# Performance work log

Measured on AMD Instinct MI355X. Metric: run time of the kernel, lower is better.

## Reference

```python
import jax, jax.numpy as jnp
import numpy as np

BETA = 0.2
ALPHA_NEG = 0.8
ALPHA_POS = 0.2
EPS = 1e-8  # torch cosine_similarity eps

B, D, P = 8192, 256, 4096


def setup_inputs() -> dict:
    key = jax.random.key(0)
    k1, k2 = jax.random.split(key)
    embeddings = jax.random.normal(k1, (B, D), dtype=jnp.float32)
    positive_pairs = jax.random.randint(k2, (P, 2), 0, B, dtype=jnp.int32)
    return {"embeddings": embeddings, "positive_pairs": positive_pairs}


def reference(embeddings, positive_pairs):
    b = embeddings.shape[0]
    p = positive_pairs.shape[0]
    # cosine similarity matrix (normalize once, single GEMM)
    nrm = jnp.maximum(jnp.linalg.norm(embeddings, axis=1, keepdims=True), EPS)
    e = embeddings / nrm
    cos = e @ e.T                              # [B, B]
    exp_cos = jnp.exp(cos / BETA)
    ii = positive_pairs[:, 0]
    jj = positive_pairs[:, 1]
    # mask = eye + positive pairs (both directions)
    mask = jnp.eye(b, dtype=bool)
    mask = mask.at[ii, jj].set(True).at[jj, ii].set(True)
    exp_masked = jnp.where(mask, 0.0, exp_cos)  # masked_fill(mask, 0)
    pos_ij = exp_cos[ii, jj]                   # [P]
    pos_ji = exp_cos[jj, ii]                   # [P]
    exp_i = exp_masked[ii]                     # [P, B]
    exp_j = exp_masked[jj]                     # [P, B]
    # hard-negative mining via alpha_neg quantile per row
    thr_i = jnp.quantile(exp_i, ALPHA_NEG, axis=1, keepdims=True)
    thr_j = jnp.quantile(exp_j, ALPHA_NEG, axis=1, keepdims=True)
    S_i = jnp.sum(jnp.where(exp_i >= thr_i, exp_i, 0.0), axis=1)  # [P]
    S_j = jnp.sum(jnp.where(exp_j >= thr_j, exp_j, 0.0), axis=1)  # [P]
    # hard-positive mining via alpha_pos quantile
    thr_pij = jnp.quantile(pos_ij, ALPHA_POS)
    thr_pji = jnp.quantile(pos_ji, ALPHA_POS)
    sel_ij = pos_ij <= thr_pij
    sel_ji = pos_ji <= thr_pji
    # torch loop zips the two (order-preserving) boolean-selected lists ->
    # truncates to min count; values are never cross-coupled, only the count.
    kmin = jnp.minimum(sel_ij.sum(), sel_ji.sum())
    act_ij = sel_ij & ((jnp.cumsum(sel_ij.astype(jnp.int32)) - 1) < kmin)
    act_ji = sel_ji & ((jnp.cumsum(sel_ji.astype(jnp.int32)) - 1) < kmin)
    # -log(pk / (pk + S[m])) = log1p(S[m] / pk), summed over all m per pk
    term_ij = jnp.log1p(S_i[None, :] / pos_ij[:, None])  # [P, P]
    term_ji = jnp.log1p(S_j[None, :] / pos_ji[:, None])  # [P, P]
    loss = (jnp.sum(term_ij * act_ij[:, None].astype(term_ij.dtype))
            + jnp.sum(term_ji * act_ji[:, None].astype(term_ji.dtype)))
    return loss / (2.0 * p)
```

## Files before the change

kernel.cpp:

```cpp
#include <hip/hip_runtime.h>
#include <stdint.h>

#define BN    8192
#define DK    256
#define PN    4096
#define MAXP  16
#define RANK_ASC 6553
#define QSTEP 0.02f

typedef float f32x4  __attribute__((ext_vector_type(4)));
typedef int   i32x4  __attribute__((ext_vector_type(4)));

__device__ __forceinline__ void gload_lds16(const void* g, void* l) {
  __builtin_amdgcn_global_load_lds(
      (const __attribute__((address_space(1))) unsigned int*)g,
      (__attribute__((address_space(3))) unsigned int*)l, 16, 0, 0);
}

__device__ __forceinline__ void find_bin_256(const unsigned* hist, int rank,
                                             int* sh, unsigned* wtot) {
  const int tid = threadIdx.x, lane = tid & 63, w = tid >> 6;
  unsigned x = hist[tid];
  unsigned pref = x;
  #pragma unroll
  for (int o = 1; o < 64; o <<= 1) {
    unsigned y = __shfl_up(pref, o);
    if (lane >= o) pref += y;
  }
  if (lane == 63) wtot[w] = pref;
  __syncthreads();
  unsigned woff = 0;
  for (int i = 0; i < w; ++i) woff += wtot[i];
  unsigned incl = pref + woff, excl = incl - x;
  if ((unsigned)rank >= excl && (unsigned)rank < incl) { sh[0] = tid; sh[1] = rank - (int)excl; }
  __syncthreads();
}

__device__ __forceinline__ float block_sum4(float x, float* red4) {
  const int lane = threadIdx.x & 63, w = threadIdx.x >> 6;
  #pragma unroll
  for (int o = 32; o; o >>= 1) x += __shfl_xor(x, o);
  __syncthreads();
  if (lane == 0) red4[w] = x;
  __syncthreads();
  return red4[0] + red4[1] + red4[2] + red4[3];
}

__global__ void __launch_bounds__(256) norm_pairs_kernel(
    const float* __restrict__ X, signed char* __restrict__ Ei8,
    const int2* __restrict__ pairs, int* pcount, int* partners,
    int* rowlist, int* cnt) {
  const int tid  = threadIdx.x;
  const int lane = tid & 63;
  const int wib  = tid >> 6;
  const int row  = blockIdx.x * 4 + wib;

  float4 x = ((const float4*)(X + (size_t)row * DK))[lane];
  float ss = x.x * x.x + x.y * x.y + x.z * x.z + x.w * x.w;
  #pragma unroll
  for (int o = 32; o; o >>= 1) ss += __shfl_xor(ss, o);
  float inv = 127.0f / fmaxf(sqrtf(ss), 1e-8f);
  int c0 = (int)rintf(inv * x.x);
  int c1 = (int)rintf(inv * x.y);
  int c2 = (int)rintf(inv * x.z);
  int c3 = (int)rintf(inv * x.w);
  unsigned u = (unsigned)(c0 & 255) | ((unsigned)(c1 & 255) << 8)
             | ((unsigned)(c2 & 255) << 16) | ((unsigned)(c3 & 255) << 24);
  ((unsigned*)(Ei8 + (size_t)row * DK))[lane] = u;

  const int p = blockIdx.x * 256 + tid;
  if (p < PN) {
    int2 pr = pairs[p];
    int ix = atomicAdd(&pcount[pr.x], 1);
    if (ix == 0) { int q = atomicAdd(cnt, 1); rowlist[q] = pr.x; }
    if (ix < MAXP) partners[pr.x * MAXP + ix] = pr.y;
    int iy = atomicAdd(&pcount[pr.y], 1);
    if (iy == 0) { int q = atomicAdd(cnt, 1); rowlist[q] = pr.y; }
    if (iy < MAXP) partners[pr.y * MAXP + iy] = pr.x;
  }
}

__global__ void __launch_bounds__(256) pos_kernel(
    const signed char* __restrict__ Ei8, const int2* __restrict__ pairs,
    float* __restrict__ pos) {
  const int tid  = threadIdx.x;
  const int lane = tid & 63;
  const int wib  = tid >> 6;
  const int p    = blockIdx.x * 4 + wib;
  int2 pr = pairs[p];
  int a = ((const int*)(Ei8 + (size_t)pr.x * DK))[lane];
  int b = ((const int*)(Ei8 + (size_t)pr.y * DK))[lane];
  int s = 0;
  #pragma unroll
  for (int j = 0; j < 4; ++j) {
    int va = (int)(signed char)(a >> (8 * j));
    int vb = (int)(signed char)(b >> (8 * j));
    s += va * vb;
  }
  #pragma unroll
  for (int o = 32; o; o >>= 1) s += __shfl_xor(s, o);
  if (lane == 0) pos[p] = __expf((float)s * (5.0f / 16129.0f));
}

__global__ void __launch_bounds__(256) gemm_code_kernel(
    const signed char* __restrict__ Ei8, const int* __restrict__ rowlist,
    const int* __restrict__ countp, uint32_t* __restrict__ out4) {
  if ((int)blockIdx.y * 128 >= *countp) return;
  __shared__ __align__(16) signed char sA[128 * 128];
  __shared__ __align__(16) signed char sB[128 * 128];
  const int tid  = threadIdx.x;
  const int lane = tid & 63;
  const int w    = tid >> 6;
  const int wm   = w >> 1, wn = w & 1;
  const int trow = blockIdx.y * 128;
  const int tcol = blockIdx.x * 128;

  const int srow = tid >> 3;
  const int sl   = tid & 7;
  const int sg   = sl ^ (srow & 7);
  int garow[4], gbrow[4];
  #pragma unroll
  for (int ii = 0; ii < 4; ++ii) {
    garow[ii] = rowlist[trow + ii * 32 + srow];
    gbrow[ii] = tcol + ii * 32 + srow;
  }

  i32x4 acc[4][4];
  #pragma unroll
  for (int i = 0; i < 4; ++i)
    #pragma unroll
    for (int j = 0; j < 4; ++j) {
      i32x4 z = {0, 0, 0, 0};
      acc[i][j] = z;
    }

  for (int kt = 0; kt < 2; ++kt) {
    const int k0 = kt * 128;
    __syncthreads();
    #pragma unroll
    for (int ii = 0; ii < 4; ++ii) {
      gload_lds16(Ei8 + (size_t)garow[ii] * DK + k0 + sg * 16, &sA[ii * 4096 + tid * 16]);
      gload_lds16(Ei8 + (size_t)gbrow[ii] * DK + k0 + sg * 16, &sB[ii * 4096 + tid * 16]);
    }
    __syncthreads();
    #pragma unroll
    for (int h = 0; h < 2; ++h) {
      const int fg = h * 4 + (lane >> 4);
      i32x4 af[4], bfg[4];
      #pragma unroll
      for (int q = 0; q < 4; ++q) {
        const int ra = wm * 64 + q * 16 + (lane & 15);
        const int rb = wn * 64 + q * 16 + (lane & 15);
        af[q]  = *(const i32x4*)&sA[ra * 128 + (fg ^ (ra & 7)) * 16];
        bfg[q] = *(const i32x4*)&sB[rb * 128 + (fg ^ (rb & 7)) * 16];
      }
      #pragma unroll
      for (int i = 0; i < 4; ++i)
        #pragma unroll
        for (int j = 0; j < 4; ++j)
          acc[i][j] = __builtin_amdgcn_mfma_i32_16x16x64_i8(af[i], bfg[j], acc[i][j], 0, 0, 0);
    }
  }

  const int crow = trow + wm * 64 + (lane >> 4) * 4;
  const int ccol = tcol + wn * 64 + (lane & 15);
  const float SCL = 250.0f / 16129.0f;
  #pragma unroll
  for (int i = 0; i < 4; ++i) {
    const int gidx = (crow + i * 16) >> 2;
    #pragma unroll
    for (int j = 0; j < 4; ++j) {
      const int col = ccol + j * 16;
      uint32_t u = 0;
      #pragma unroll
      for (int r = 0; r < 4; ++r) {
        int c = (int)fmaf((float)acc[i][j][r], SCL, 128.5f);
        c = c < 1 ? 1 : (c > 255 ? 255 : c);
        u |= (uint32_t)c << (8 * r);
      }
      out4[(size_t)gidx * BN + col] = u;
    }
  }
}

__global__ void __launch_bounds__(256) row_stats4_kernel(
    const uint32_t* __restrict__ expc4, const int* __restrict__ rowlist,
    const int* __restrict__ countp, const int* __restrict__ pcount,
    const int* __restrict__ partners, float* __restrict__ S) {
  __shared__ unsigned hist[4][4][256];
  __shared__ unsigned total[4][256];
  __shared__ int plist[4][MAXP + 1];
  __shared__ int npl[4];
  __shared__ int growl[4];
  __shared__ int sh[2];
  __shared__ unsigned wtot[4];
  __shared__ float redf[4];
  const int g = blockIdx.x;
  const int cnt = *countp;
  if (g * 4 >= cnt) return;
  const int tid = threadIdx.x, lane = tid & 63, w = tid >> 6;

  uint4 rv[8];
  const uint4* src = (const uint4*)(expc4 + (size_t)g * BN);
  #pragma unroll
  for (int q = 0; q < 8; ++q) rv[q] = src[q * 256 + tid];

  if (tid < 4) {
    int rr = g * 4 + tid;
    int grow = (rr < cnt) ? rowlist[rr] : -1;
    growl[tid] = grow;
    int np = 0;
    if (grow >= 0) {
      np = pcount[grow]; if (np > MAXP) np = MAXP;
      for (int e = 0; e < np; ++e) plist[tid][e] = partners[grow * MAXP + e];
      plist[tid][np] = grow;
      np++;
    }
    npl[tid] = np;
  }
  #pragma unroll
  for (int k = 0; k < 16; ++k) ((unsigned*)hist)[k * 256 + tid] = 0;
  __syncthreads();

  #pragma unroll
  for (int r4 = 0; r4 < 4; ++r4) {
    const int np = npl[r4];
    for (int e = 0; e < np; ++e) {
      int c = plist[r4][e];
      int t = c >> 2;
      if ((t & 255) == tid) {
        unsigned* wp = (unsigned*)&rv[t >> 8];
        wp[c & 3] &= ~(0xFFu << (r4 * 8));
      }
    }
  }

  unsigned* h = (unsigned*)hist[w];
  #pragma unroll
  for (int q = 0; q < 8; ++q) {
    #pragma unroll
    for (int word = 0; word < 4; ++word) {
      unsigned dw = ((const unsigned*)&rv[q])[word];
      atomicAdd(&h[0 * 256 + (dw & 255u)], 1u);
      atomicAdd(&h[1 * 256 + ((dw >> 8) & 255u)], 1u);
      atomicAdd(&h[2 * 256 + ((dw >> 16) & 255u)], 1u);
      atomicAdd(&h[3 * 256 + (dw >> 24)], 1u);
    }
  }
  __syncthreads();
  #pragma unroll
  for (int r4 = 0; r4 < 4; ++r4)
    total[r4][tid] = hist[0][r4][tid] + hist[1][r4][tid] + hist[2][r4][tid] + hist[3][r4][tid];
  __syncthreads();

  const float val = __expf((float)(tid - 128) * QSTEP);
  for (int r4 = 0; r4 < 4; ++r4) {
    find_bin_256(total[r4], RANK_ASC, sh, wtot);
    const int b    = sh[0];
    const int need = (int)total[r4][b] - sh[1];
    float contrib = (tid > b) ? (float)total[r4][tid] * val
                  : (tid == b) ? (float)need * val : 0.f;
    #pragma unroll
    for (int o = 32; o; o >>= 1) contrib += __shfl_xor(contrib, o);
    __syncthreads();
    if (lane == 0) redf[w] = contrib;
    __syncthreads();
    if (tid == 0 && growl[r4] >= 0)
      S[growl[r4]] = redf[0] + redf[1] + redf[2] + redf[3];
    __syncthreads();
  }
}

__global__ void __launch_bounds__(256) finale_kernel(
    const float* __restrict__ pos, const int2* __restrict__ pairs,
    const float* __restrict__ S, float* __restrict__ out) {
  __shared__ uint32_t v[PN];
  __shared__ unsigned hist[256];
  __shared__ int sh[2];
  __shared__ unsigned wtot[4];
  __shared__ float red4[4];
  const int tid = threadIdx.x;
  for (int i = tid; i < PN; i += 256) v[i] = ((const uint32_t*)pos)[i];
  __syncthreads();
  int rank = 819;
  uint32_t prefix = 0;
  for (int pass = 0; pass < 4; ++pass) {
    const int shift = 24 - pass * 8;
    hist[tid] = 0;
    __syncthreads();
    for (int i = tid; i < PN; i += 256) {
      uint32_t x = v[i];
      bool match = (pass == 0) || ((x >> (shift + 8)) == (prefix >> (shift + 8)));
      if (match) atomicAdd(&hist[(x >> shift) & 255u], 1u);
    }
    __syncthreads();
    find_bin_256(hist, rank, sh, wtot);
    prefix |= ((uint32_t)sh[0]) << shift;
    rank = sh[1];
    __syncthreads();
  }
  float thr; __builtin_memcpy(&thr, &prefix, 4);

  float n = 0.f, sl = 0.f, sp = 0.f, sp2 = 0.f;
  for (int r = tid; r < PN; r += 256) {
    float p; uint32_t b = v[r]; __builtin_memcpy(&p, &b, 4);
    if (p <= thr) { n += 1.f; sl += __logf(p); sp += p; sp2 += p * p; }
  }
  float t = 0.f, u = 0.f, vv = 0.f;
  for (int c = tid; c < PN; c += 256) {
    int2 pr = pairs[c];
    float s1 = S[pr.x], s2 = S[pr.y];
    float i1 = 1.f / s1, i2 = 1.f / s2;
    t += __logf(s1) + __logf(s2);
    u += i1 + i2;
    vv += i1 * i1 + i2 * i2;
  }
  const float N   = block_sum4(n, red4);
  const float SL  = block_sum4(sl, red4);
  const float SP  = block_sum4(sp, red4);
  const float SP2 = block_sum4(sp2, red4);
  const float T   = block_sum4(t, red4);
  const float U   = block_sum4(u, red4);
  const float V   = block_sum4(vv, red4);
  if (tid == 0) {
    double num = (double)N * T - 2.0 * (double)PN * (double)SL
               + (double)SP * U - 0.5 * (double)SP2 * V;
    out[0] = (float)(num / (2.0 * (double)PN));
  }
}

extern "C" void kernel_launch(void* const* d_in, const int* in_sizes, int n_in,
                              void* d_out, int out_size, void* d_ws, size_t ws_size,
                              hipStream_t stream) {
  const float* emb  = (const float*)d_in[0];
  const int2* pairs = (const int2*)d_in[1];
  float* out = (float*)d_out;

  char* w = (char*)d_ws;
  size_t off = 0;
  int*         pcnt  = (int*)(w + off);         off += (size_t)BN * 4;
  int*         rlist = (int*)(w + off);         off += (size_t)BN * 4;
  int*         cnt   = (int*)(w + off);         off += 256;
  signed char* Ei8   = (signed char*)(w + off); off += (size_t)BN * DK;
  float*       S     = (float*)(w + off);       off += (size_t)BN * 4;
  float*       pos   = (float*)(w + off);       off += (size_t)PN * 4;
  int*         parts = (int*)(w + off);         off += (size_t)BN * MAXP * 4;
  uint32_t*    out4  = (uint32_t*)(w + off);    off += (size_t)(BN / 4) * BN * 4;

  hipMemsetAsync(pcnt, 0, (size_t)BN * 8 + 256, stream);
  norm_pairs_kernel<<<BN / 4, 256, 0, stream>>>(emb, Ei8, pairs, pcnt, parts, rlist, cnt);
  pos_kernel<<<PN / 4, 256, 0, stream>>>(Ei8, pairs, pos);
  gemm_code_kernel<<<dim3(BN / 128, BN / 128), 256, 0, stream>>>(Ei8, rlist, cnt, out4);
  row_stats4_kernel<<<BN / 4, 256, 0, stream>>>(out4, rlist, cnt, pcnt, parts, S);
  finale_kernel<<<1, 256, 0, stream>>>(pos, pairs, S, out);
}
```

Before: 148.3 us.

## Fuse finale into row-stats kernel via last-block atomic and use nontemporal stores/loads

The separate single-block finale kernel is removed. Its work now runs at the end of row_stats4_kernel, in whichever block is last to increment an atomic done counter, with thread fences around the handoff. The GEMM output codes are written with nontemporal stores and read back with nontemporal loads to limit cache pollution. This saves one kernel launch and its gap, at the cost of an atomic and fences in every block. It also relies on the memset zeroing the done counter, which sits inside the cleared region next to cnt.

```diff
diff --git a/kernel.cpp b/kernel.cpp
--- a/kernel.cpp
+++ b/kernel.cpp
@@ -8,8 +8,9 @@
 #define RANK_ASC 6553
 #define QSTEP 0.02f
 
-typedef float f32x4  __attribute__((ext_vector_type(4)));
-typedef int   i32x4  __attribute__((ext_vector_type(4)));
+typedef float    f32x4 __attribute__((ext_vector_type(4)));
+typedef int      i32x4 __attribute__((ext_vector_type(4)));
+typedef unsigned u32x4 __attribute__((ext_vector_type(4)));
 
 __device__ __forceinline__ void gload_lds16(const void* g, void* l) {
   __builtin_amdgcn_global_load_lds(
@@ -178,7 +179,7 @@
         c = c < 1 ? 1 : (c > 255 ? 255 : c);
         u |= (uint32_t)c << (8 * r);
       }
-      out4[(size_t)gidx * BN + col] = u;
+      __builtin_nontemporal_store(u, &out4[(size_t)gidx * BN + col]);
     }
   }
 }
@@ -186,7 +187,9 @@
 __global__ void __launch_bounds__(256) row_stats4_kernel(
     const uint32_t* __restrict__ expc4, const int* __restrict__ rowlist,
     const int* __restrict__ countp, const int* __restrict__ pcount,
-    const int* __restrict__ partners, float* __restrict__ S) {
+    const int* __restrict__ partners, float* __restrict__ S,
+    int* done, const float* __restrict__ pos, const int2* __restrict__ pairs,
+    float* __restrict__ out) {
   __shared__ unsigned hist[4][4][256];
   __shared__ unsigned total[4][256];
   __shared__ int plist[4][MAXP + 1];
@@ -198,12 +201,13 @@
   const int g = blockIdx.x;
   const int cnt = *countp;
   if (g * 4 >= cnt) return;
+  const int nact = (cnt + 3) >> 2;
   const int tid = threadIdx.x, lane = tid & 63, w = tid >> 6;
 
-  uint4 rv[8];
-  const uint4* src = (const uint4*)(expc4 + (size_t)g * BN);
-  #pragma unroll
-  for (int q = 0; q < 8; ++q) rv[q] = src[q * 256 + tid];
+  u32x4 rv[8];
+  const u32x4* src = (const u32x4*)(expc4 + (size_t)g * BN);
+  #pragma unroll
+  for (int q = 0; q < 8; ++q) rv[q] = __builtin_nontemporal_load(&src[q * 256 + tid]);
 
   if (tid < 4) {
     int rr = g * 4 + tid;
@@ -269,42 +273,44 @@
       S[growl[r4]] = redf[0] + redf[1] + redf[2] + redf[3];
     __syncthreads();
   }
-}
-
-__global__ void __launch_bounds__(256) finale_kernel(
-    const float* __restrict__ pos, const int2* __restrict__ pairs,
-    const float* __restrict__ S, float* __restrict__ out) {
-  __shared__ uint32_t v[PN];
-  __shared__ unsigned hist[256];
-  __shared__ int sh[2];
-  __shared__ unsigned wtot[4];
-  __shared__ float red4[4];
-  const int tid = threadIdx.x;
-  for (int i = tid; i < PN; i += 256) v[i] = ((const uint32_t*)pos)[i];
+
+  if (tid == 0) {
+    __threadfence();
+    int old = atomicAdd(done, 1);
+    sh[0] = (old == nact - 1) ? 1 : 0;
+  }
+  __syncthreads();
+  if (!sh[0]) return;
+  __threadfence();
+
+  unsigned* v     = (unsigned*)hist;
+  unsigned* fhist = total[0];
+  __syncthreads();
+  for (int i = tid; i < PN; i += 256) v[i] = ((const unsigned*)pos)[i];
   __syncthreads();
   int rank = 819;
   uint32_t prefix = 0;
   for (int pass = 0; pass < 4; ++pass) {
     const int shift = 24 - pass * 8;
-    hist[tid] = 0;
+    fhist[tid] = 0;
     __syncthreads();
     for (int i = tid; i < PN; i += 256) {
       uint32_t x = v[i];
       bool match = (pass == 0) || ((x >> (shift + 8)) == (prefix >> (shift + 8)));
-      if (match) atomicAdd(&hist[(x >> shift) & 255u], 1u);
-    }
-    __syncthreads();
-    find_bin_256(hist, rank, sh, wtot);
+      if (match) atomicAdd(&fhist[(x >> shift) & 255u], 1u);
+    }
+    __syncthreads();
+    find_bin_256(fhist, rank, sh, wtot);
     prefix |= ((uint32_t)sh[0]) << shift;
     rank = sh[1];
     __syncthreads();
   }
   float thr; __builtin_memcpy(&thr, &prefix, 4);
 
-  float n = 0.f, sl = 0.f, sp = 0.f, sp2 = 0.f;
+  float n = 0.f, slg = 0.f, sp = 0.f, sp2 = 0.f;
   for (int r = tid; r < PN; r += 256) {
     float p; uint32_t b = v[r]; __builtin_memcpy(&p, &b, 4);
-    if (p <= thr) { n += 1.f; sl += __logf(p); sp += p; sp2 += p * p; }
+    if (p <= thr) { n += 1.f; slg += __logf(p); sp += p; sp2 += p * p; }
   }
   float t = 0.f, u = 0.f, vv = 0.f;
   for (int c = tid; c < PN; c += 256) {
@@ -315,13 +321,13 @@
     u += i1 + i2;
     vv += i1 * i1 + i2 * i2;
   }
-  const float N   = block_sum4(n, red4);
-  const float SL  = block_sum4(sl, red4);
-  const float SP  = block_sum4(sp, red4);
-  const float SP2 = block_sum4(sp2, red4);
-  const float T   = block_sum4(t, red4);
-  const float U   = block_sum4(u, red4);
-  const float V   = block_sum4(vv, red4);
+  const float N   = block_sum4(n, redf);
+  const float SL  = block_sum4(slg, redf);
+  const float SP  = block_sum4(sp, redf);
+  const float SP2 = block_sum4(sp2, redf);
+  const float T   = block_sum4(t, redf);
+  const float U   = block_sum4(u, redf);
+  const float V   = block_sum4(vv, redf);
   if (tid == 0) {
     double num = (double)N * T - 2.0 * (double)PN * (double)SL
                + (double)SP * U - 0.5 * (double)SP2 * V;
@@ -346,11 +352,12 @@
   float*       pos   = (float*)(w + off);       off += (size_t)PN * 4;
   int*         parts = (int*)(w + off);         off += (size_t)BN * MAXP * 4;
   uint32_t*    out4  = (uint32_t*)(w + off);    off += (size_t)(BN / 4) * BN * 4;
+  int*         done  = cnt + 1;
 
   hipMemsetAsync(pcnt, 0, (size_t)BN * 8 + 256, stream);
   norm_pairs_kernel<<<BN / 4, 256, 0, stream>>>(emb, Ei8, pairs, pcnt, parts, rlist, cnt);
   pos_kernel<<<PN / 4, 256, 0, stream>>>(Ei8, pairs, pos);
   gemm_code_kernel<<<dim3(BN / 128, BN / 128), 256, 0, stream>>>(Ei8, rlist, cnt, out4);
-  row_stats4_kernel<<<BN / 4, 256, 0, stream>>>(out4, rlist, cnt, pcnt, parts, S);
-  finale_kernel<<<1, 256, 0, stream>>>(pos, pairs, S, out);
-}
+  row_stats4_kernel<<<BN / 4, 256, 0, stream>>>(out4, rlist, cnt, pcnt, parts, S,
+                                                done, pos, pairs, out);
+}
```

Result: slower. 171.6 us (+15.6%).
